# Performance work log

Measured on AMD Instinct MI355X. Metric: run time of the kernel, lower is better.

## Reference

```python
import jax, jax.numpy as jnp
import numpy as np

HIDDEN = 3072
N_HEADS = 16
Q_LORA = 1536
KV_LORA = 512
NOPE = 128
ROPE = 64
QK_HD = NOPE + ROPE  # 192
V_HD = 128
B, S = 2, 1024


def rms_norm(x, w, eps=1e-6):
    xf = x.astype(jnp.float32)
    var = jnp.mean(xf * xf, axis=-1, keepdims=True)
    return w * (xf * jax.lax.rsqrt(var + eps)).astype(x.dtype)


def apply_rope(x):
    # x: (b, s, h, d) with d even; interleaved pair rotation as in the source
    b, s, h, d = x.shape
    pos = jnp.arange(s, dtype=jnp.float32)
    inv_freq = 1.0 / (10000.0 ** (jnp.arange(0, d, 2, dtype=jnp.float32) / d))
    ang = pos[:, None] * inv_freq[None, :]          # (s, d/2)
    sin = jnp.sin(ang)[None, :, None, :]            # (1, s, 1, d/2)
    cos = jnp.cos(ang)[None, :, None, :]
    xr = x.reshape(b, s, h, d // 2, 2)
    x1, x2 = xr[..., 0], xr[..., 1]
    r1 = x1 * cos - x2 * sin
    r2 = x1 * sin + x2 * cos
    return jnp.stack([r1, r2], axis=-1).reshape(b, s, h, d)


def setup_inputs() -> dict:
    key = jax.random.key(0)
    ks = jax.random.split(key, 16)
    sc = 0.02
    inp = {
        "hidden_states": jax.random.normal(ks[0], (B, S, HIDDEN), jnp.float32),
        # causal additive mask (s, t): 0 on/below diagonal, -1e9 above
        "mask": jnp.where(jnp.tril(jnp.ones((S, S), bool)), 0.0, -1e9).astype(jnp.float32),
        "wq_a_w": jax.random.normal(ks[1], (Q_LORA, HIDDEN), jnp.float32) * sc,
        "wq_a_b": jnp.zeros((Q_LORA,), jnp.float32),
        "q_norm_w": jnp.ones((Q_LORA,), jnp.float32),
        "wq_b_w": jax.random.normal(ks[2], (HIDDEN, Q_LORA), jnp.float32) * sc,
        "wq_b_b": jnp.zeros((HIDDEN,), jnp.float32),
        "wkv_a_w": jax.random.normal(ks[3], (KV_LORA + ROPE, HIDDEN), jnp.float32) * sc,
        "wkv_a_b": jnp.zeros((KV_LORA + ROPE,), jnp.float32),
        "kv_norm_w": jnp.ones((KV_LORA,), jnp.float32),
        "wkv_b_w": jax.random.normal(ks[4], (N_HEADS * (NOPE + V_HD), KV_LORA), jnp.float32) * sc,
        "wkv_b_b": jnp.zeros((N_HEADS * (NOPE + V_HD),), jnp.float32),
        "wo_w": jax.random.normal(ks[5], (HIDDEN, N_HEADS * V_HD), jnp.float32) * sc,
        "wo_b": jnp.zeros((HIDDEN,), jnp.float32),
    }
    return inp


def reference(hidden_states, mask, wq_a_w, wq_a_b, q_norm_w, wq_b_w, wq_b_b,
              wkv_a_w, wkv_a_b, kv_norm_w, wkv_b_w, wkv_b_b, wo_w, wo_b):
    b, s, _ = hidden_states.shape
    scale = QK_HD ** (-0.5)

    # low-rank Q projection
    q_lat = hidden_states @ wq_a_w.T + wq_a_b                  # (b,s,q_lora)
    q = rms_norm(q_lat, q_norm_w) @ wq_b_w.T + wq_b_b          # (b,s,hidden)
    q = q.reshape(b, s, N_HEADS, QK_HD)
    q_nope, q_rope = q[..., :NOPE], q[..., NOPE:]
    q_rope = apply_rope(q_rope)
    q = jnp.concatenate([q_nope, q_rope], axis=-1)             # (b,s,h,192)

    # low-rank KV projection with decoupled rope key
    kv = hidden_states @ wkv_a_w.T + wkv_a_b                   # (b,s,kv_lora+rope)
    kv_lat, k_rope = kv[..., :KV_LORA], kv[..., KV_LORA:]
    k_rope = apply_rope(k_rope[:, :, None, :])                 # (b,s,1,64)
    kv = rms_norm(kv_lat, kv_norm_w) @ wkv_b_w.T + wkv_b_b
    kv = kv.reshape(b, s, N_HEADS, NOPE + V_HD)
    k_nope, v = kv[..., :NOPE], kv[..., NOPE:]
    k = jnp.concatenate([k_nope, jnp.broadcast_to(k_rope, (b, s, N_HEADS, ROPE))], axis=-1)

    # naive full attention, fp32 softmax (as in source)
    scores = jnp.einsum('bshd,bthd->bsht', q, k) * scale       # (b,s,h,t)
    scores = scores + mask[None, :, None, :]
    p = jax.nn.softmax(scores.astype(jnp.float32), axis=-1)
    out = jnp.einsum('bsht,bthd->bshd', p, v)                  # (b,s,h,v_hd)
    out = out.reshape(b, s, N_HEADS * V_HD)
    return out @ wo_w.T + wo_b
```

## Files before the change

### kernel.cpp

```cpp
#include <hip/hip_runtime.h>
#include <stdint.h>
#include <stddef.h>

#define NHEADS 16
#define QLORA  1536
#define KVLORA 512
#define QKH    192
#define VH     128
#define BB     2
#define SS     1024
#define MROWS  (BB*SS)
#define HID    3072

typedef __attribute__((ext_vector_type(4))) float fx4;
typedef __attribute__((ext_vector_type(4))) short sx4;
typedef __attribute__((ext_vector_type(8))) short sx8;

__device__ __forceinline__ short f2bf(float f) {
  uint32_t u = __builtin_bit_cast(uint32_t, f);
  u = (u + 0x7fffu + ((u >> 16) & 1u)) >> 16;
  return (short)u;
}
__device__ __forceinline__ float bf2f(short s) {
  uint32_t u = ((uint32_t)(uint16_t)s) << 16;
  return __builtin_bit_cast(float, u);
}
__device__ __forceinline__ void gl_lds16(const void* g, void* l) {
  __builtin_amdgcn_global_load_lds((const __attribute__((address_space(1))) void*)g,
                                   (__attribute__((address_space(3))) void*)l, 16, 0, 0);
}
__device__ __forceinline__ sx8 ldfrag(const short* p) {
  sx4 lo = *(const sx4*)p;
  sx4 hi = *(const sx4*)(p + 16);
  sx8 r;
  r[0]=lo[0]; r[1]=lo[1]; r[2]=lo[2]; r[3]=lo[3];
  r[4]=hi[0]; r[5]=hi[1]; r[6]=hi[2]; r[7]=hi[3];
  return r;
}
__device__ __forceinline__ sx8 ldfrag_swz(const short* lds, int row, int rowShorts,
                                          int baseChunk, int g) {
  const int r7 = row & 7;
  const int gh = g >> 1, lo4 = (g & 1) * 4;
  int ch0 = baseChunk + gh;
  int ch1 = baseChunk + 2 + gh;
  ch0 = (ch0 & ~7) | ((ch0 & 7) ^ r7);
  ch1 = (ch1 & ~7) | ((ch1 & 7) ^ r7);
  const short* base = lds + row * rowShorts;
  sx4 a = *(const sx4*)(base + ch0 * 8 + lo4);
  sx4 b = *(const sx4*)(base + ch1 * 8 + lo4);
  sx8 r;
  r[0]=a[0]; r[1]=a[1]; r[2]=a[2]; r[3]=a[3];
  r[4]=b[0]; r[5]=b[1]; r[6]=b[2]; r[7]=b[3];
  return r;
}

struct CvtSeg { const float* src; short* dst; int n4; };
__device__ __forceinline__ void cvt_one(const CvtSeg& sg, int i) {
  fx4 v = *(const fx4*)(sg.src + (size_t)i * 4);
  sx4 o;
  o[0] = f2bf(v[0]); o[1] = f2bf(v[1]); o[2] = f2bf(v[2]); o[3] = f2bf(v[3]);
  *(sx4*)(sg.dst + (size_t)i * 4) = o;
}

__global__ void k_cvt3(CvtSeg s0, CvtSeg s1, CvtSeg s2, float* __restrict__ tab) {
  if ((int)blockIdx.x >= 1024) {
    int i = ((int)blockIdx.x - 1024) * 256 + threadIdx.x;
    if (i < SS * 32) {
      int pos = i >> 5, fi = i & 31;
      float inv = powf(10000.0f, -(float)fi / 32.0f);
      float ang = (float)pos * inv;
      tab[i * 2]     = cosf(ang);
      tab[i * 2 + 1] = sinf(ang);
    }
    return;
  }
  const CvtSeg segs[3] = {s0, s1, s2};
  const int stride = 1024 * 256;
  const int t0 = blockIdx.x * 256 + threadIdx.x;
#pragma unroll
  for (int s = 0; s < 3; ++s)
    for (int i = t0; i < segs[s].n4; i += stride) cvt_one(segs[s], i);
}

struct GemmProb {
  const short* A; const short* Bt; const float* bias; void* C;
  int N; int K;
};

template <int MFR, int SPLITK>
__global__ __launch_bounds__(256, 2)
void k_gemmS(GemmProb p0, GemmProb p1, int nblk0, int nbGemm,
             CvtSeg c0, CvtSeg c1) {
  if ((int)blockIdx.x >= nbGemm) {
    const int nthr = ((int)gridDim.x - nbGemm) * 256;
    const int t0 = ((int)blockIdx.x - nbGemm) * 256 + threadIdx.x;
    if (c0.src) for (int i = t0; i < c0.n4; i += nthr) cvt_one(c0, i);
    if (c1.src) for (int i = t0; i < c1.n4; i += nthr) cvt_one(c1, i);
    return;
  }
  constexpr int TM = MFR * 32;
  constexpr int MT = 2048 / TM;
  int bid = ((int)blockIdx.x % 8) * (nbGemm >> 3) + ((int)blockIdx.x >> 3);
  const GemmProb p = (bid < nblk0) ? p0 : p1;
  int lb = (bid < nblk0) ? bid : bid - nblk0;
  const int N = p.N, K = p.K;
  const int NT = (N + 127) >> 7;
  const int tiles = MT * NT;
  const int tile = lb % tiles;
  const int pi = (SPLITK > 1) ? (lb / tiles) : 0;
  const int m0 = (tile % MT) * TM;
  const int n0 = (tile / MT) * 128;
  const int Kc = K / SPLITK;
  const int k0 = pi * Kc;

  __shared__ short As[TM * 64];
  __shared__ short Bs[128 * 64];
  const int tid  = threadIdx.x;
  const int lane = tid & 63;
  const int g    = lane >> 4;
  const int r16  = lane & 15;
  const int wave = tid >> 6;
  const int wm   = (wave >> 1) * (TM / 2);
  const int wn   = (wave & 1) * 64;

  fx4 acc[MFR][4] = {};

  for (int kk = k0; kk < k0 + Kc; kk += 64) {
#pragma unroll
    for (int i = 0; i < MFR; ++i) {
      int cc  = tid + 256 * i;
      int row = cc >> 3;
      int src = ((cc & 7) ^ (row & 7)) * 8;
      gl_lds16(p.A + (size_t)(m0 + row) * K + kk + src, &As[cc * 8]);
    }
#pragma unroll
    for (int i = 0; i < 4; ++i) {
      int cc  = tid + 256 * i;
      int row = cc >> 3;
      int src = ((cc & 7) ^ (row & 7)) * 8;
      int bn = n0 + row; if (bn > N - 1) bn = N - 1;
      gl_lds16(p.Bt + (size_t)bn * K + kk + src, &Bs[cc * 8]);
    }
    __syncthreads();

#pragma unroll
    for (int s = 0; s < 2; ++s) {
      sx8 bfv[4];
#pragma unroll
      for (int ni = 0; ni < 4; ++ni)
        bfv[ni] = ldfrag_swz(Bs, wn + ni * 16 + r16, 64, s * 4, g);
#pragma unroll
      for (int mi = 0; mi < MFR; ++mi) {
        sx8 af = ldfrag_swz(As, wm + mi * 16 + r16, 64, s * 4, g);
#pragma unroll
        for (int ni = 0; ni < 4; ++ni)
          acc[mi][ni] = __builtin_amdgcn_mfma_f32_16x16x32_bf16(af, bfv[ni], acc[mi][ni], 0, 0, 0);
      }
    }
    __syncthreads();
  }

  if (SPLITK > 1) {
    short* Cp = (short*)p.C + (size_t)pi * 2048 * N;
#pragma unroll
    for (int mi = 0; mi < MFR; ++mi) {
      int mbase = m0 + wm + mi * 16 + 4 * g;
#pragma unroll
      for (int ni = 0; ni < 4; ++ni) {
        int ncol = n0 + wn + ni * 16 + r16;
        if (ncol < N) {
#pragma unroll
          for (int r = 0; r < 4; ++r)
            Cp[(size_t)(mbase + r) * N + ncol] = f2bf(acc[mi][ni][r]);
        }
      }
    }
  } else {
#pragma unroll
    for (int mi = 0; mi < MFR; ++mi) {
      int mbase = m0 + wm + mi * 16 + 4 * g;
#pragma unroll
      for (int ni = 0; ni < 4; ++ni) {
        int ncol = n0 + wn + ni * 16 + r16;
        if (ncol < N) {
          float bv = p.bias[ncol];
#pragma unroll
          for (int r = 0; r < 4; ++r)
            ((short*)p.C)[(size_t)(mbase + r) * N + ncol] = f2bf(acc[mi][ni][r] + bv);
        }
      }
    }
  }
}

__global__ __launch_bounds__(256)
void k_prep(const short* __restrict__ qp, const float* __restrict__ q_bias,
            const float* __restrict__ q_norm_w, short* __restrict__ qn,
            const short* __restrict__ kvp, const float* __restrict__ kv_bias,
            const float* __restrict__ kv_norm_w, short* __restrict__ kvn,
            short* __restrict__ kr, const float* __restrict__ tab) {
  const int row = blockIdx.x;
  const int t = threadIdx.x;
  const size_t QS = (size_t)2048 * QLORA;
  const size_t KS = (size_t)2048 * 576;

  float x[8];
  float s1 = 0.f, s2 = 0.f;
  if (t < 192) {
    const short* a = qp + (size_t)row * QLORA + t * 8;
    sx8 u = *(const sx8*)(a);
    sx8 v = *(const sx8*)(a + QS);
    sx8 w = *(const sx8*)(a + 2 * QS);
#pragma unroll
    for (int j = 0; j < 8; ++j) {
      x[j] = bf2f(u[j]) + bf2f(v[j]) + bf2f(w[j]) + q_bias[t * 8 + j];
      s1 += x[j] * x[j];
    }
  } else {
    const int c = t - 192;
    const short* a = kvp + (size_t)row * 576 + c * 8;
    sx8 u = *(const sx8*)(a);
    sx8 v = *(const sx8*)(a + KS);
    sx8 w = *(const sx8*)(a + 2 * KS);
#pragma unroll
    for (int j = 0; j < 8; ++j) {
      x[j] = bf2f(u[j]) + bf2f(v[j]) + bf2f(w[j]) + kv_bias[c * 8 + j];
      s2 += x[j] * x[j];
    }
  }
#pragma unroll
  for (int o = 32; o >= 1; o >>= 1) {
    s1 += __shfl_xor(s1, o, 64);
    s2 += __shfl_xor(s2, o, 64);
  }
  __shared__ float r1[4], r2[4];
  if ((t & 63) == 0) { r1[t >> 6] = s1; r2[t >> 6] = s2; }
  __syncthreads();
  float qss = r1[0] + r1[1] + r1[2] + r1[3];
  float kss = r2[0] + r2[1] + r2[2] + r2[3];
  float qrs = 1.0f / sqrtf(qss / (float)QLORA + 1e-6f);
  float krs = 1.0f / sqrtf(kss / (float)KVLORA + 1e-6f);

  if (t < 192) {
    sx8 o;
#pragma unroll
    for (int j = 0; j < 8; ++j) o[j] = f2bf(x[j] * qrs * q_norm_w[t * 8 + j]);
    *(sx8*)(qn + (size_t)row * QLORA + t * 8) = o;
  } else {
    int c = t - 192;
    sx8 o;
#pragma unroll
    for (int j = 0; j < 8; ++j) o[j] = f2bf(x[j] * krs * kv_norm_w[c * 8 + j]);
    *(sx8*)(kvn + (size_t)row * KVLORA + c * 8) = o;
  }
  if (t < 8) {
    const short* a = kvp + (size_t)row * 576 + 512 + t * 8;
    sx8 u = *(const sx8*)(a);
    sx8 v = *(const sx8*)(a + KS);
    sx8 w = *(const sx8*)(a + 2 * KS);
    float y[8];
#pragma unroll
    for (int j = 0; j < 8; ++j)
      y[j] = bf2f(u[j]) + bf2f(v[j]) + bf2f(w[j]) + kv_bias[512 + t * 8 + j];
    int pos = row & (SS - 1);
    sx8 o;
#pragma unroll
    for (int k = 0; k < 4; ++k) {
      int i = t * 4 + k;
      float c = tab[(pos * 32 + i) * 2], s = tab[(pos * 32 + i) * 2 + 1];
      o[2 * k]     = f2bf(y[2 * k] * c - y[2 * k + 1] * s);
      o[2 * k + 1] = f2bf(y[2 * k] * s + y[2 * k + 1] * c);
    }
    *(sx8*)(kr + (size_t)row * 64 + t * 8) = o;
  }
}

__global__ __launch_bounds__(256)
void k_post(const short* __restrict__ kvb, short* __restrict__ vt,
            short* __restrict__ qb, const float* __restrict__ tab) {
  const int bid = blockIdx.x;
  const int tid = threadIdx.x;
  if (bid < 512) {
    const int bh = bid >> 4;
    const int t0 = (bid & 15) * 64;
    const int b = bh >> 4, h = bh & 15;
    __shared__ short sm[64 * 128];
#pragma unroll
    for (int i = 0; i < 4; ++i) {
      int c = tid + 256 * i;
      int tt = c >> 4, d0 = (c & 15) * 8;
      sx8 v = *(const sx8*)(kvb + ((size_t)(b * SS + t0 + tt)) * 4096 + h * 256 + 128 + d0);
      *(sx8*)(sm + tt * 128 + d0) = v;
    }
    __syncthreads();
#pragma unroll
    for (int i = 0; i < 4; ++i) {
      int c = tid + 256 * i;
      int d = c >> 3, tof = (c & 7) * 8;
      sx8 v;
#pragma unroll
      for (int j = 0; j < 8; ++j) v[j] = sm[(tof + j) * 128 + d];
      *(sx8*)(vt + ((size_t)bh * VH + d) * SS + t0 + tof) = v;
    }
  } else {
    int p = (bid - 512) * 256 + tid;
    int j = p & 7, h = (p >> 3) & 15, row = p >> 7;
    int pos = row & (SS - 1);
    size_t base = (((size_t)row * NHEADS + h) * QKH) + 128 + j * 8;
    sx8 x = *(const sx8*)(qb + base);
    sx8 o;
#pragma unroll
    for (int k = 0; k < 4; ++k) {
      int i = j * 4 + k;
      float c = tab[(pos * 32 + i) * 2], s = tab[(pos * 32 + i) * 2 + 1];
      float x1 = bf2f(x[2 * k]), x2 = bf2f(x[2 * k + 1]);
      o[2 * k]     = f2bf(x1 * c - x2 * s);
      o[2 * k + 1] = f2bf(x1 * s + x2 * c);
    }
    *(sx8*)(qb + base) = o;
  }
}

__global__ __launch_bounds__(256)
void k_osum(const short* __restrict__ p, const float* __restrict__ bias,
            float* __restrict__ out) {
  const size_t OS = (size_t)2048 * HID;
  int i = blockIdx.x * 256 + threadIdx.x;
  sx8 a = *(const sx8*)(p + (size_t)i * 8);
  sx8 b = *(const sx8*)(p + OS + (size_t)i * 8);
  int col = (i * 8) % HID;
  fx4 o0, o1;
#pragma unroll
  for (int j = 0; j < 4; ++j) {
    o0[j] = bf2f(a[j]) + bf2f(b[j]) + bias[col + j];
    o1[j] = bf2f(a[4 + j]) + bf2f(b[4 + j]) + bias[col + 4 + j];
  }
  *(fx4*)(out + (size_t)i * 8) = o0;
  *(fx4*)(out + (size_t)i * 8 + 4) = o1;
}

__global__ __launch_bounds__(256, 2)
void k_attn(const short* __restrict__ q, const short* __restrict__ kvb,
            const short* __restrict__ kr, const short* __restrict__ vt,
            short* __restrict__ ao) {
  const int bh = blockIdx.x;
  const int b = bh >> 4, h = bh & 15;
  const int py = blockIdx.y;
  const int qi = (py < 8) ? py : 23 - py;
  const int qt0 = qi * 64;
  const int tid = threadIdx.x;
  const int lane = tid & 63;
  const int wave = tid >> 6;
  const int g = lane >> 4, r16 = lane & 15;
  const int qg = qt0 + wave * 16 + r16;

  __shared__ short Ks[64 * QKH];
  __shared__ short Vs[VH * 64];

  sx8 qf[6];
  {
    const short* qr = q + (((size_t)(b * SS + qg)) * NHEADS + h) * QKH;
#pragma unroll
    for (int f = 0; f < 6; ++f) qf[f] = ldfrag(qr + f * 32 + 4 * g);
  }

  float mrun = -1e30f, lrun = 0.0f;
  fx4 oacc[8] = {};
  const float scale = 0.07216878364870323f;

  const int ntiles = qt0 / 64 + 1;
  for (int kt = 0; kt < ntiles; ++kt) {
    const int t0 = kt * 64;
#pragma unroll
    for (int i = 0; i < 6; ++i) {
      int cc = tid + 256 * i;
      int row = cc / 24, ch = cc % 24;
      int sc = (ch & 24) | ((ch & 7) ^ (row & 7));
      size_t grow = (size_t)(b * SS + t0 + row);
      const short* src = (sc < 16) ? kvb + grow * 4096 + h * 256 + sc * 8
                                   : kr + grow * 64 + (sc - 16) * 8;
      gl_lds16(src, &Ks[cc * 8]);
    }
#pragma unroll
    for (int i = 0; i < 4; ++i) {
      int cc = tid + 256 * i;
      int row = cc >> 3;
      int sc = (cc & 7) ^ (row & 7);
      gl_lds16(vt + ((size_t)bh * VH + row) * SS + t0 + sc * 8, &Vs[cc * 8]);
    }
    __syncthreads();

    const bool diag = (kt == ntiles - 1);
    float pv[16];
    float tmax = -1e30f;
#pragma unroll
    for (int th = 0; th < 4; ++th) {
      fx4 sacc = {};
#pragma unroll
      for (int f = 0; f < 6; ++f) {
        sx8 kf = ldfrag_swz(Ks, th * 16 + r16, QKH, f * 4, g);
        sacc = __builtin_amdgcn_mfma_f32_16x16x32_bf16(kf, qf[f], sacc, 0, 0, 0);
      }
#pragma unroll
      for (int r = 0; r < 4; ++r) {
        int t = t0 + th * 16 + 4 * g + r;
        float s = sacc[r] * scale;
        if (diag && t > qg) s = -1e30f;
        pv[th * 4 + r] = s;
        tmax = fmaxf(tmax, s);
      }
    }
    tmax = fmaxf(tmax, __shfl_xor(tmax, 16, 64));
    tmax = fmaxf(tmax, __shfl_xor(tmax, 32, 64));
    float mnew = fmaxf(mrun, tmax);
    float corr = __expf(mrun - mnew);
    float psum = 0.f;
#pragma unroll
    for (int j = 0; j < 16; ++j) { pv[j] = __expf(pv[j] - mnew); psum += pv[j]; }
    psum += __shfl_xor(psum, 16, 64);
    psum += __shfl_xor(psum, 32, 64);
    lrun = lrun * corr + psum;
    mrun = mnew;
#pragma unroll
    for (int f8 = 0; f8 < 8; ++f8) oacc[f8] *= corr;

    sx8 pf0, pf1;
#pragma unroll
    for (int j = 0; j < 8; ++j) { pf0[j] = f2bf(pv[j]); pf1[j] = f2bf(pv[8 + j]); }

#pragma unroll
    for (int f8 = 0; f8 < 8; ++f8) {
      sx8 v0 = ldfrag_swz(Vs, f8 * 16 + r16, 64, 0, g);
      sx8 v1 = ldfrag_swz(Vs, f8 * 16 + r16, 64, 4, g);
      oacc[f8] = __builtin_amdgcn_mfma_f32_16x16x32_bf16(v0, pf0, oacc[f8], 0, 0, 0);
      oacc[f8] = __builtin_amdgcn_mfma_f32_16x16x32_bf16(v1, pf1, oacc[f8], 0, 0, 0);
    }
    __syncthreads();
  }

  float inv = 1.0f / lrun;
#pragma unroll
  for (int f8 = 0; f8 < 8; ++f8)
#pragma unroll
    for (int r = 0; r < 4; ++r) {
      int d = f8 * 16 + 4 * g + r;
      ao[(((size_t)(b * SS + qg)) * NHEADS + h) * VH + d] = f2bf(oacc[f8][r] * inv);
    }
}

extern "C" void kernel_launch(void* const* d_in, const int* in_sizes, int n_in,
                              void* d_out, int out_size, void* d_ws, size_t ws_size,
                              hipStream_t stream) {
  const float* hs       = (const float*)d_in[0];
  const float* wq_a_w   = (const float*)d_in[2];
  const float* wq_a_b   = (const float*)d_in[3];
  const float* q_norm_w = (const float*)d_in[4];
  const float* wq_b_w   = (const float*)d_in[5];
  const float* wq_b_b   = (const float*)d_in[6];
  const float* wkv_a_w  = (const float*)d_in[7];
  const float* wkv_a_b  = (const float*)d_in[8];
  const float* kv_norm_w= (const float*)d_in[9];
  const float* wkv_b_w  = (const float*)d_in[10];
  const float* wkv_b_b  = (const float*)d_in[11];
  const float* wo_w     = (const float*)d_in[12];
  const float* wo_b     = (const float*)d_in[13];
  float* out = (float*)d_out;

  short* ws0 = (short*)d_ws;
  size_t off = 0;
  short* wqa_bf  = ws0 + off; off += (size_t)QLORA * HID;
  short* wqb_bf  = ws0 + off; off += (size_t)HID * QLORA;
  short* wkva_bf = ws0 + off; off += (size_t)576 * HID;
  short* wkvb_bf = ws0 + off; off += (size_t)4096 * KVLORA;
  short* wo_bf   = ws0 + off; off += (size_t)HID * 2048;
  short* h_bf    = ws0 + off; off += (size_t)MROWS * HID;
  short* qn      = ws0 + off; off += (size_t)MROWS * QLORA;
  short* kvn     = ws0 + off; off += (size_t)MROWS * KVLORA;
  short* kr      = ws0 + off; off += (size_t)MROWS * 64;
  short* qb      = ws0 + off; off += (size_t)MROWS * HID;
  short* kvb     = ws0 + off; off += (size_t)MROWS * 4096;
  short* vtb     = ws0 + off; off += (size_t)BB * NHEADS * VH * SS;
  short* ao      = ws0 + off; off += (size_t)MROWS * 2048;
  float* tab     = (float*)(ws0 + off + (off & 1));
  short* arena   = (short*)(tab + SS * 64);
  short* qlatp   = arena;
  short* kvp     = arena + (size_t)3 * 2048 * QLORA;
  short* wop     = arena;

  {
    CvtSeg s0{hs,      h_bf,    (int)((size_t)MROWS * HID / 4)};
    CvtSeg s1{wq_a_w,  wqa_bf,  (int)((size_t)QLORA * HID / 4)};
    CvtSeg s2{wkv_a_w, wkva_bf, (int)((size_t)576 * HID / 4)};
    k_cvt3<<<1024 + 128, 256, 0, stream>>>(s0, s1, s2, tab);
  }

  {
    GemmProb pq{h_bf, wqa_bf,  nullptr, qlatp, QLORA, HID};
    GemmProb pk{h_bf, wkva_bf, nullptr, kvp,   576,   HID};
    int nb0 = 8 * (QLORA / 128) * 3;
    int nb1 = 8 * ((576 + 127) / 128) * 3;
    int nbG = nb0 + nb1;
    CvtSeg c0{wq_b_w,  wqb_bf,  (int)((size_t)HID * QLORA / 4)};
    CvtSeg c1{wkv_b_w, wkvb_bf, (int)((size_t)4096 * KVLORA / 4)};
    k_gemmS<8, 3><<<nbG + 192, 256, 0, stream>>>(pq, pk, nb0, nbG, c0, c1);
  }

  k_prep<<<MROWS, 256, 0, stream>>>(qlatp, wq_a_b, q_norm_w, qn,
                                    kvp, wkv_a_b, kv_norm_w, kvn, kr, tab);

  {
    GemmProb pq{qn,  wqb_bf,  wq_b_b,  qb,  HID,  QLORA};
    GemmProb pk{kvn, wkvb_bf, wkv_b_b, kvb, 4096, KVLORA};
    int nb0 = 8 * (HID / 128);
    int nb1 = 8 * (4096 / 128);
    int nbG = nb0 + nb1;
    CvtSeg c0{wo_w, wo_bf, (int)((size_t)HID * 2048 / 4)};
    CvtSeg c1{nullptr, nullptr, 0};
    k_gemmS<8, 1><<<nbG + 192, 256, 0, stream>>>(pq, pk, nb0, nbG, c0, c1);
  }

  k_post<<<512 + 1024, 256, 0, stream>>>(kvb, vtb, qb, tab);

  k_attn<<<dim3(BB * NHEADS, SS / 64), 256, 0, stream>>>(qb, kvb, kr, vtb, ao);

  {
    GemmProb po{ao, wo_bf, nullptr, wop, HID, 2048};
    int nb = 8 * (HID / 128) * 2;
    CvtSeg cz{nullptr, nullptr, 0};
    k_gemmS<8, 2><<<nb, 256, 0, stream>>>(po, po, nb, nb, cz, cz);
  }
  k_osum<<<(MROWS * HID / 8) / 256, 256, 0, stream>>>(wop, wo_b, out);
}
```

Before: 230.8 us.

## Double-buffer GEMM LDS tiles with K-step 32 and raise occupancy

The GEMM kernel now uses two LDS buffers of half depth (K=32 per stage), with a new swizzle and fragment loader. It prefetches the next stage while the MFMAs consume the current one, replacing the load-sync-compute-sync pattern, and raises the launch bound minimum to 3 blocks per SM. Each loop iteration now does fewer MFMAs per barrier, and the higher occupancy target may force register spills. The MFR/2 loop assumes MFR is even.

Result: slower. 356.9 us (+54.7%).

```diff
diff --git a/kernel.cpp b/kernel.cpp
--- a/kernel.cpp
+++ b/kernel.cpp
@@ -53,6 +53,19 @@
   r[4]=b[0]; r[5]=b[1]; r[6]=b[2]; r[7]=b[3];
   return r;
 }
+__device__ __forceinline__ sx8 ldfrag_swz32(const short* lds, int row, int g) {
+  const int f = (row >> 1) & 3;
+  const int c0 = (g >> 1) ^ f;
+  const int c1 = (2 + (g >> 1)) ^ f;
+  const int lo4 = (g & 1) * 4;
+  const short* base = lds + row * 32;
+  sx4 a = *(const sx4*)(base + c0 * 8 + lo4);
+  sx4 b = *(const sx4*)(base + c1 * 8 + lo4);
+  sx8 r;
+  r[0]=a[0]; r[1]=a[1]; r[2]=a[2]; r[3]=a[3];
+  r[4]=b[0]; r[5]=b[1]; r[6]=b[2]; r[7]=b[3];
+  return r;
+}
 
 struct CvtSeg { const float* src; short* dst; int n4; };
 __device__ __forceinline__ void cvt_one(const CvtSeg& sg, int i) {
@@ -88,7 +101,7 @@
 };
 
 template <int MFR, int SPLITK>
-__global__ __launch_bounds__(256, 2)
+__global__ __launch_bounds__(256, 3)
 void k_gemmS(GemmProb p0, GemmProb p1, int nblk0, int nbGemm,
              CvtSeg c0, CvtSeg c1) {
   if ((int)blockIdx.x >= nbGemm) {
@@ -113,8 +126,8 @@
   const int Kc = K / SPLITK;
   const int k0 = pi * Kc;
 
-  __shared__ short As[TM * 64];
-  __shared__ short Bs[128 * 64];
+  __shared__ short As[2][TM * 32];
+  __shared__ short Bs[2][128 * 32];
   const int tid  = threadIdx.x;
   const int lane = tid & 63;
   const int g    = lane >> 4;
@@ -125,40 +138,50 @@
 
   fx4 acc[MFR][4] = {};
 
-  for (int kk = k0; kk < k0 + Kc; kk += 64) {
-#pragma unroll
-    for (int i = 0; i < MFR; ++i) {
-      int cc  = tid + 256 * i;
-      int row = cc >> 3;
-      int src = ((cc & 7) ^ (row & 7)) * 8;
-      gl_lds16(p.A + (size_t)(m0 + row) * K + kk + src, &As[cc * 8]);
-    }
-#pragma unroll
-    for (int i = 0; i < 4; ++i) {
-      int cc  = tid + 256 * i;
-      int row = cc >> 3;
-      int src = ((cc & 7) ^ (row & 7)) * 8;
-      int bn = n0 + row; if (bn > N - 1) bn = N - 1;
-      gl_lds16(p.Bt + (size_t)bn * K + kk + src, &Bs[cc * 8]);
-    }
-    __syncthreads();
-
-#pragma unroll
-    for (int s = 0; s < 2; ++s) {
+#define STAGE(bufi, kk)                                                        \
+  do {                                                                         \
+    _Pragma("unroll")                                                          \
+    for (int i = 0; i < MFR / 2; ++i) {                                        \
+      int cc = tid + 256 * i;                                                  \
+      int row = cc >> 2;                                                       \
+      int sc = ((cc & 3) ^ (row >> 1)) & 3;                                    \
+      gl_lds16(p.A + (size_t)(m0 + row) * K + (kk) + sc * 8,                   \
+               &As[bufi][cc * 8]);                                             \
+    }                                                                          \
+    _Pragma("unroll")                                                          \
+    for (int i = 0; i < 2; ++i) {                                              \
+      int cc = tid + 256 * i;                                                  \
+      int row = cc >> 2;                                                       \
+      int sc = ((cc & 3) ^ (row >> 1)) & 3;                                    \
+      int bn = n0 + row; if (bn > N - 1) bn = N - 1;                           \
+      gl_lds16(p.Bt + (size_t)bn * K + (kk) + sc * 8, &Bs[bufi][cc * 8]);      \
+    }                                                                          \
+  } while (0)
+
+  const int nk = Kc >> 5;
+  STAGE(0, k0);
+  __syncthreads();
+
+  int cur = 0;
+  for (int t = 0; t < nk; ++t) {
+    if (t + 1 < nk) STAGE(cur ^ 1, k0 + (t + 1) * 32);
+    {
       sx8 bfv[4];
 #pragma unroll
       for (int ni = 0; ni < 4; ++ni)
-        bfv[ni] = ldfrag_swz(Bs, wn + ni * 16 + r16, 64, s * 4, g);
+        bfv[ni] = ldfrag_swz32(&Bs[cur][0], wn + ni * 16 + r16, g);
 #pragma unroll
       for (int mi = 0; mi < MFR; ++mi) {
-        sx8 af = ldfrag_swz(As, wm + mi * 16 + r16, 64, s * 4, g);
+        sx8 af = ldfrag_swz32(&As[cur][0], wm + mi * 16 + r16, g);
 #pragma unroll
         for (int ni = 0; ni < 4; ++ni)
           acc[mi][ni] = __builtin_amdgcn_mfma_f32_16x16x32_bf16(af, bfv[ni], acc[mi][ni], 0, 0, 0);
       }
     }
     __syncthreads();
-  }
+    cur ^= 1;
+  }
+#undef STAGE
 
   if (SPLITK > 1) {
     short* Cp = (short*)p.C + (size_t)pi * 2048 * N;
```
